# Optimization experiments

Measured on AMD Instinct MI355X. Metric: run time of the kernel, lower is better.

Reference implementation:

```python
import jax, jax.numpy as jnp
import numpy as np

N = 50000      # nodes
E = 1600000    # edges (avg degree 32)
F_IN = 128
HID = 256
C = 40


def setup_inputs() -> dict:
    key = jax.random.key(0)
    ks = jax.random.split(key, 12)
    x = jax.random.normal(ks[0], (N, F_IN), jnp.float32)
    edge_index = jax.random.randint(ks[1], (2, E), 0, N, dtype=jnp.int32)

    def glorot(k, fan_in, fan_out):
        s = jnp.sqrt(2.0 / (fan_in + fan_out)).astype(jnp.float32)
        return jax.random.normal(k, (fan_in, fan_out), jnp.float32) * s

    return {
        "x": x,
        "edge_index": edge_index,
        "W1": glorot(ks[2], F_IN, HID), "b1": jnp.zeros((HID,), jnp.float32),
        "W2": glorot(ks[3], HID, HID),  "b2": jnp.zeros((HID,), jnp.float32),
        "W3": glorot(ks[4], HID, HID),  "b3": jnp.zeros((HID,), jnp.float32),
        "W4": glorot(ks[5], HID, C),    "b4": jnp.zeros((C,), jnp.float32),
    }


def _gcn_conv(x, W, b, src, dst, norm_e, self_norm):
    # PyG GCNConv: h = X W; out_j = sum_i norm_ij * h_i  (+ self-loop term) + b
    h = x @ W                                   # [N, F_out]
    msg = h[src] * norm_e[:, None]              # [E, F_out] gather + scale
    agg = jax.ops.segment_sum(msg, dst, num_segments=N)
    agg = agg + h * self_norm[:, None]          # self-loop contribution
    return agg + b


def reference(x, edge_index, W1, b1, W2, b2, W3, b3, W4, b4):
    src, dst = edge_index[0], edge_index[1]
    # degree on A + I (self-loops added), computed over destination nodes
    deg = jax.ops.segment_sum(jnp.ones((E,), x.dtype), dst, num_segments=N) + 1.0
    inv_sqrt = jax.lax.rsqrt(deg)               # [N]
    norm_e = inv_sqrt[src] * inv_sqrt[dst]      # [E] symmetric norm per edge
    self_norm = inv_sqrt * inv_sqrt             # [N] self-loop norm = 1/deg

    h = jax.nn.relu(_gcn_conv(x, W1, b1, src, dst, norm_e, self_norm))
    h = jax.nn.relu(_gcn_conv(h, W2, b2, src, dst, norm_e, self_norm))
    h = jax.nn.relu(_gcn_conv(h, W3, b3, src, dst, norm_e, self_norm))
    h = _gcn_conv(h, W4, b4, src, dst, norm_e, self_norm)
    return jax.nn.log_softmax(h, axis=1)
```

## Files before the change

### kernel.cpp

```cpp
#include <hip/hip_runtime.h>
#include <hip/hip_fp16.h>
#include <math.h>


typedef _Float16 f16x8 __attribute__((ext_vector_type(8)));
typedef float f32x4 __attribute__((ext_vector_type(4)));
typedef unsigned u32x4 __attribute__((ext_vector_type(4)));

#define CAP 80

#define AS1 __attribute__((address_space(1)))
#define AS3 __attribute__((address_space(3)))

__device__ __forceinline__ void dma16(const unsigned short* g,
                                      const unsigned short* ldsBase) {
    __builtin_amdgcn_global_load_lds((const AS1 void*)(size_t)g,
                                     (AS3 void*)(unsigned)(size_t)ldsBase,
                                     16, 0, 0);
}

__device__ __forceinline__ __half2 u2h2(unsigned u) {
    union { unsigned u; __half2 h; } v; v.u = u; return v.h;
}
__device__ __forceinline__ unsigned h22u(__half2 h) {
    union { unsigned u; __half2 h; } v; v.h = h; return v.u;
}
__device__ __forceinline__ float hlo(unsigned u) {
    return __half2float(__ushort_as_half((unsigned short)(u & 0xFFFFu)));
}
__device__ __forceinline__ float hhi(unsigned u) {
    return __half2float(__ushort_as_half((unsigned short)(u >> 16)));
}

__global__ __launch_bounds__(256) void count_prep_kernel(
        const int* __restrict__ dst,
        int* __restrict__ cnt, int* __restrict__ rank, int E, int nEdgeBlocks,
        const float* __restrict__ x, unsigned short* __restrict__ xb, int nx4,
        const float* __restrict__ W1, const float* __restrict__ W2,
        const float* __restrict__ W3, const float* __restrict__ W4,
        unsigned short* __restrict__ Wt1, unsigned short* __restrict__ Wt2,
        unsigned short* __restrict__ Wt3, unsigned short* __restrict__ Wt4) {
    int b = blockIdx.x;
    if (b < nEdgeBlocks) {
        int e = b * 256 + threadIdx.x;
        if (e < E) rank[e] = atomicAdd(&cnt[dst[e]], 1);
        return;
    }
    int i = (b - nEdgeBlocks) * 256 + threadIdx.x;
    if (i < nx4) {
        float4 v = reinterpret_cast<const float4*>(x)[i];
        ushort4 o;
        o.x = __half_as_ushort(__float2half_rn(v.x));
        o.y = __half_as_ushort(__float2half_rn(v.y));
        o.z = __half_as_ushort(__float2half_rn(v.z));
        o.w = __half_as_ushort(__float2half_rn(v.w));
        reinterpret_cast<ushort4*>(xb)[i] = o;
        return;
    }
    int j = i - nx4;
    if (j < 32768) {
        int k = j >> 8, n = j & 255;
        Wt1[n * 128 + k] = __half_as_ushort(__float2half_rn(W1[j]));
    } else if (j < 98304) {
        int t = j - 32768; int k = t >> 8, n = t & 255;
        Wt2[n * 256 + k] = __half_as_ushort(__float2half_rn(W2[t]));
    } else if (j < 163840) {
        int t = j - 98304; int k = t >> 8, n = t & 255;
        Wt3[n * 256 + k] = __half_as_ushort(__float2half_rn(W3[t]));
    } else if (j < 174080) {
        int t = j - 163840; int k = t / 40, n = t - k * 40;
        Wt4[n * 256 + k] = __half_as_ushort(__float2half_rn(W4[t]));
    }
}

__global__ __launch_bounds__(256) void scatter_rsq_kernel(
        const int* __restrict__ src, const int* __restrict__ dst,
        const int* __restrict__ rank, unsigned short* __restrict__ epk,
        int E, int nEdgeBlocks,
        const int* __restrict__ cnt, float* __restrict__ rsq, int N) {
    int b = blockIdx.x;
    if (b < nEdgeBlocks) {
        int e = b * 256 + threadIdx.x;
        if (e < E) {
            int d = dst[e];
            int s = src[e];
            int r = rank[e]; if (r >= CAP) r = CAP - 1;
            epk[(size_t)d * CAP + r] = (unsigned short)s;
        }
        return;
    }
    int n = (b - nEdgeBlocks) * 256 + threadIdx.x;
    if (n < N) rsq[n] = rsqrtf((float)cnt[n] + 1.0f);
}

template <int ROWB, bool WSRC, bool BIAS, bool RELU>
__global__ __launch_bounds__(256) void agg_wide_kernel(
        const unsigned short* __restrict__ G,
        const int* __restrict__ cnt,
        const unsigned short* __restrict__ epk,
        const float* __restrict__ rsq,
        const float* __restrict__ bias,
        unsigned short* __restrict__ out, int N) {
    constexpr int ROWS = ROWB / 2;
    constexpr int LPN = ROWB / 16;
    constexpr int LOG_LPN = (LPN == 32) ? 5 : 4;
    constexpr int NPW = 64 / LPN;
    int lane = threadIdx.x & 63;
    int wid = threadIdx.x >> 6;
    int sub = lane >> LOG_LPN;
    int off = lane & (LPN - 1);
    int node = blockIdx.x * (4 * NPW) + wid * NPW + sub;
    if (node >= N) return;

    const unsigned short* gb = G + off * 8;
    const unsigned short* ep = epk + (size_t)node * CAP;
    int deg = cnt[node]; if (deg > CAP) deg = CAP;

    __half2 acc[4];
    #pragma unroll
    for (int k = 0; k < 4; k++) acc[k] = u2h2(0u);

    int e = 0;
    for (; e + 7 < deg; e += 8) {
        uint4 pv = *reinterpret_cast<const uint4*>(ep + e);
        int s[8];
        s[0] = pv.x & 0xFFFFu; s[1] = pv.x >> 16;
        s[2] = pv.y & 0xFFFFu; s[3] = pv.y >> 16;
        s[4] = pv.z & 0xFFFFu; s[5] = pv.z >> 16;
        s[6] = pv.w & 0xFFFFu; s[7] = pv.w >> 16;
        uint4 v[8];
        #pragma unroll
        for (int j = 0; j < 8; j++)
            v[j] = *reinterpret_cast<const uint4*>(gb + (size_t)s[j] * ROWS);
        if (WSRC) {
            float ws[8];
            #pragma unroll
            for (int j = 0; j < 8; j++) ws[j] = rsq[s[j]];
            #pragma unroll
            for (int j = 0; j < 8; j++) {
                __half2 w2 = __half2half2(__float2half_rn(ws[j]));
                acc[0] = __hfma2(w2, u2h2(v[j].x), acc[0]);
                acc[1] = __hfma2(w2, u2h2(v[j].y), acc[1]);
                acc[2] = __hfma2(w2, u2h2(v[j].z), acc[2]);
                acc[3] = __hfma2(w2, u2h2(v[j].w), acc[3]);
            }
        } else {
            #pragma unroll
            for (int j = 0; j < 8; j++) {
                acc[0] = __hadd2(acc[0], u2h2(v[j].x));
                acc[1] = __hadd2(acc[1], u2h2(v[j].y));
                acc[2] = __hadd2(acc[2], u2h2(v[j].z));
                acc[3] = __hadd2(acc[3], u2h2(v[j].w));
            }
        }
    }
    for (; e < deg; e++) {
        int s0 = ep[e];
        uint4 v0 = *reinterpret_cast<const uint4*>(gb + (size_t)s0 * ROWS);
        if (WSRC) {
            __half2 w2 = __half2half2(__float2half_rn(rsq[s0]));
            acc[0] = __hfma2(w2, u2h2(v0.x), acc[0]);
            acc[1] = __hfma2(w2, u2h2(v0.y), acc[1]);
            acc[2] = __hfma2(w2, u2h2(v0.z), acc[2]);
            acc[3] = __hfma2(w2, u2h2(v0.w), acc[3]);
        } else {
            acc[0] = __hadd2(acc[0], u2h2(v0.x));
            acc[1] = __hadd2(acc[1], u2h2(v0.y));
            acc[2] = __hadd2(acc[2], u2h2(v0.z));
            acc[3] = __hadd2(acc[3], u2h2(v0.w));
        }
    }

    float r = rsq[node];
    uint4 sv = *reinterpret_cast<const uint4*>(gb + (size_t)node * ROWS);
    unsigned svu[4] = {sv.x, sv.y, sv.z, sv.w};
    float sw = WSRC ? r : 1.0f;
    float r2 = r * r;
    u32x4 wp;
    float4 bv0, bv1;
    if (!WSRC && BIAS) {
        bv0 = reinterpret_cast<const float4*>(bias)[off * 2];
        bv1 = reinterpret_cast<const float4*>(bias)[off * 2 + 1];
    }
    float bvf[8] = {bv0.x, bv0.y, bv0.z, bv0.w, bv1.x, bv1.y, bv1.z, bv1.w};
    #pragma unroll
    for (int k = 0; k < 4; k++) {
        float2 f = __half22float2(acc[k]);
        f.x = fmaf(sw, hlo(svu[k]), f.x);
        f.y = fmaf(sw, hhi(svu[k]), f.y);
        float ox, oy;
        if (WSRC) {
            ox = r * f.x; oy = r * f.y;
        } else {
            ox = r2 * f.x; oy = r2 * f.y;
            if (BIAS) {
                ox = fmaf(r, bvf[2 * k], ox);
                oy = fmaf(r, bvf[2 * k + 1], oy);
            }
            if (RELU) { ox = fmaxf(ox, 0.f); oy = fmaxf(oy, 0.f); }
        }
        wp[k] = h22u(__floats2half2_rn(ox, oy));
    }
    __builtin_nontemporal_store(
        wp, reinterpret_cast<u32x4*>(out + (size_t)node * ROWS + off * 8));
}

__global__ __launch_bounds__(256) void agg40_softmax_kernel(
        const unsigned* __restrict__ G,
        const int* __restrict__ cnt,
        const unsigned short* __restrict__ epk,
        const float* __restrict__ rsq,
        const float* __restrict__ bias,
        float* __restrict__ out, int N) {
    int lane = threadIdx.x & 63;
    int node = blockIdx.x * 4 + (threadIdx.x >> 6);
    if (node >= N) return;
    bool act = lane < 20;
    int cl = act ? lane : 0;
    const unsigned short* ep = epk + (size_t)node * CAP;
    int deg = cnt[node]; if (deg > CAP) deg = CAP;
    __half2 acch = u2h2(0u);
    int e = 0;
    for (; e + 7 < deg; e += 8) {
        uint4 pv = *reinterpret_cast<const uint4*>(ep + e);
        int s[8];
        s[0] = pv.x & 0xFFFFu; s[1] = pv.x >> 16;
        s[2] = pv.y & 0xFFFFu; s[3] = pv.y >> 16;
        s[4] = pv.z & 0xFFFFu; s[5] = pv.z >> 16;
        s[6] = pv.w & 0xFFFFu; s[7] = pv.w >> 16;
        unsigned g[8];
        #pragma unroll
        for (int j = 0; j < 8; j++) g[j] = G[(size_t)s[j] * 20 + cl];
        #pragma unroll
        for (int j = 0; j < 8; j++) acch = __hadd2(acch, u2h2(g[j]));
    }
    for (; e < deg; e++) {
        int s0 = ep[e];
        acch = __hadd2(acch, u2h2(G[(size_t)s0 * 20 + cl]));
    }
    float lo = 0.f, hi = 0.f;
    if (act) {
        float r = rsq[node];
        unsigned sv = G[(size_t)node * 20 + lane];
        float2 f = __half22float2(acch);
        f.x += hlo(sv); f.y += hhi(sv);
        lo = fmaf(r, f.x, bias[2 * lane]);
        hi = fmaf(r, f.y, bias[2 * lane + 1]);
    }
    float m = act ? fmaxf(lo, hi) : -INFINITY;
    #pragma unroll
    for (int o = 32; o >= 1; o >>= 1) m = fmaxf(m, __shfl_xor(m, o, 64));
    float s = act ? (expf(lo - m) + expf(hi - m)) : 0.f;
    #pragma unroll
    for (int o = 32; o >= 1; o >>= 1) s += __shfl_xor(s, o, 64);
    float ls = logf(s);
    if (act) {
        float2 o2;
        o2.x = lo - m - ls;
        o2.y = hi - m - ls;
        *reinterpret_cast<float2*>(out + (size_t)node * 40 + 2 * lane) = o2;
    }
}

template <int BK, bool BIAS, bool RELU, bool SCALE>
__global__ __launch_bounds__(256) void gemm_f16(
        const unsigned short* __restrict__ A,
        const unsigned short* __restrict__ Bt,
        const float* __restrict__ bias,
        const float* __restrict__ rsqRow,
        unsigned short* __restrict__ Cout,
        int M, int K, int Nc) {
    constexpr int SPR = BK / 8;
    constexpr int NSTG = (128 * SPR) / 256;
    __shared__ __align__(16) unsigned short As[128 * BK];
    __shared__ __align__(16) unsigned short Bs[128 * BK];
    int tid = threadIdx.x;
    int lane = tid & 63;
    int wid = tid >> 6;
    int rowBase = blockIdx.y * 128;
    int colBase = blockIdx.x * 128;
    int waveM = (wid & 1) * 64;
    int waveN = (wid >> 1) * 64;

    f32x4 acc[4][4] = {};
    int lrow = lane & 15;
    int kgrp = (lane >> 4) * 8;

    for (int k0 = 0; k0 < K; k0 += BK) {
        #pragma unroll
        for (int c = 0; c < NSTG; c++) {
            int base16 = c * 256 + wid * 64;
            int slot = base16 + lane;
            int row = slot / SPR;
            int kp = (slot % SPR) * 8;
            int ksw = kp ^ ((row & (SPR - 1)) * 8);
            int gr = rowBase + row; if (gr >= M) gr = M - 1;
            dma16(A + (size_t)gr * K + k0 + ksw, &As[base16 * 8]);
            int gc = colBase + row; if (gc >= Nc) gc = Nc - 1;
            dma16(Bt + (size_t)gc * K + k0 + ksw, &Bs[base16 * 8]);
        }
        __syncthreads();
        #pragma unroll
        for (int kk = 0; kk < BK; kk += 32) {
            f16x8 af[4], bfr[4];
            #pragma unroll
            for (int t = 0; t < 4; t++) {
                int ra = waveM + t * 16 + lrow;
                af[t] = *reinterpret_cast<const f16x8*>(
                    &As[ra * BK + ((kk + kgrp) ^ ((ra & (SPR - 1)) * 8))]);
                int rb = waveN + t * 16 + lrow;
                bfr[t] = *reinterpret_cast<const f16x8*>(
                    &Bs[rb * BK + ((kk + kgrp) ^ ((rb & (SPR - 1)) * 8))]);
            }
            #pragma unroll
            for (int mt = 0; mt < 4; mt++)
                #pragma unroll
                for (int nt = 0; nt < 4; nt++)
                    acc[mt][nt] = __builtin_amdgcn_mfma_f32_16x16x32_f16(
                        af[mt], bfr[nt], acc[mt][nt], 0, 0, 0);
        }
        __syncthreads();
    }

    #pragma unroll
    for (int mt = 0; mt < 4; mt++) {
        #pragma unroll
        for (int r = 0; r < 4; r++) {
            int row = rowBase + waveM + mt * 16 + (lane >> 4) * 4 + r;
            if (row >= M) continue;
            float rs = SCALE ? rsqRow[row] : 1.0f;
            #pragma unroll
            for (int nt = 0; nt < 4; nt++) {
                int col = colBase + waveN + nt * 16 + (lane & 15);
                if (col >= Nc) continue;
                float v = acc[mt][nt][r];
                if (BIAS) v += bias[col];
                if (RELU) v = fmaxf(v, 0.f);
                if (SCALE) v *= rs;
                Cout[(size_t)row * Nc + col] = __half_as_ushort(__float2half_rn(v));
            }
        }
    }
}


extern "C" void kernel_launch(void* const* d_in, const int* in_sizes, int n_in,
                              void* d_out, int out_size, void* d_ws, size_t ws_size,
                              hipStream_t stream) {
    const float* x  = (const float*)d_in[0];
    const int*   ei = (const int*)d_in[1];
    const float* W1 = (const float*)d_in[2];
    const float* b1 = (const float*)d_in[3];
    const float* W2 = (const float*)d_in[4];
    const float* b2 = (const float*)d_in[5];
    const float* W3 = (const float*)d_in[6];
    const float* b3 = (const float*)d_in[7];
    const float* W4 = (const float*)d_in[8];
    const float* b4 = (const float*)d_in[9];

    const int FIN = 128, HID = 256, C = 40;
    const int N = in_sizes[0] / FIN;
    const int E = in_sizes[1] / 2;
    const int* src = ei;
    const int* dst = ei + E;

    char* w = (char*)d_ws;
    auto alloc = [&](size_t bytes) {
        char* p = w;
        w += (bytes + 255) & ~(size_t)255;
        return p;
    };
    int*   cnt    = (int*)alloc((size_t)N * 4);
    float* rsq    = (float*)alloc((size_t)N * 4);
    unsigned short* epk = (unsigned short*)alloc((size_t)N * CAP * 2);
    unsigned short* aggx = (unsigned short*)alloc((size_t)N * FIN * 2);
    unsigned short* bufA = (unsigned short*)alloc((size_t)N * HID * 2);
    unsigned short* bufB = (unsigned short*)alloc((size_t)N * HID * 2);
    unsigned short* Wt1 = (unsigned short*)alloc((size_t)FIN * HID * 2);
    unsigned short* Wt2 = (unsigned short*)alloc((size_t)HID * HID * 2);
    unsigned short* Wt3 = (unsigned short*)alloc((size_t)HID * HID * 2);
    unsigned short* Wt4 = (unsigned short*)alloc((size_t)HID * C * 2);
    unsigned short* xb = bufB;
    int* rank = (int*)aggx;

    hipMemsetAsync(cnt, 0, (size_t)N * 4, stream);

    int nx4 = N * FIN / 4;
    int nEdgeBlocks = (E + 255) / 256;
    int prepBlocks = (nx4 + 174080 + 255) / 256;
    count_prep_kernel<<<nEdgeBlocks + prepBlocks, 256, 0, stream>>>(
        dst, cnt, rank, E, nEdgeBlocks,
        x, xb, nx4, W1, W2, W3, W4, Wt1, Wt2, Wt3, Wt4);
    int rsqBlocks = (N + 255) / 256;
    scatter_rsq_kernel<<<nEdgeBlocks + rsqBlocks, 256, 0, stream>>>(
        src, dst, rank, epk, E, nEdgeBlocks, cnt, rsq, N);

    dim3 gAgg1((N + 15) / 16);
    dim3 gAggH((N + 7) / 8);
    int grp = (N + 3) / 4;
    dim3 gHID((HID + 127) / 128, (N + 127) / 128);
    dim3 gC((C + 127) / 128, (N + 127) / 128);

    agg_wide_kernel<256, true, false, false>
        <<<gAgg1, 256, 0, stream>>>(xb, cnt, epk, rsq, nullptr, aggx, N);
    gemm_f16<128, true, true, true><<<gHID, 256, 0, stream>>>(
        aggx, Wt1, b1, rsq, bufA, N, FIN, HID);
    gemm_f16<128, false, false, false><<<gHID, 256, 0, stream>>>(
        bufA, Wt2, nullptr, nullptr, bufB, N, HID, HID);
    agg_wide_kernel<512, false, true, true>
        <<<gAggH, 256, 0, stream>>>(bufB, cnt, epk, rsq, b2, bufA, N);
    gemm_f16<128, false, false, false><<<gHID, 256, 0, stream>>>(
        bufA, Wt3, nullptr, nullptr, bufB, N, HID, HID);
    agg_wide_kernel<512, false, true, true>
        <<<gAggH, 256, 0, stream>>>(bufB, cnt, epk, rsq, b3, bufA, N);
    gemm_f16<128, false, false, false><<<gC, 256, 0, stream>>>(
        bufA, Wt4, nullptr, nullptr, bufB, N, HID, C);
    agg40_softmax_kernel<<<grp, 256, 0, stream>>>((const unsigned*)bufB, cnt, epk,
                                                  rsq, b4, (float*)d_out, N);
}
```

Before: 577.3 us.

## Parallelize final 40-class aggregation across edges with LDS reduction

The final aggregation+log-softmax kernel previously used only 20 of 64 lanes, each gathering one half2 per edge serially. Now the wavefront processes 12 edges at once, each edge handled by 5 lanes doing 16-byte loads of the 40-half row, with per-lane partial sums reduced through shared memory. This raises memory-level parallelism and lane utilization for the gather, at the cost of an LDS round-trip and masked tail work. Summation order in fp16 changes slightly.

```diff
diff --git a/kernel.cpp b/kernel.cpp
--- a/kernel.cpp
+++ b/kernel.cpp
@@ -206,42 +206,51 @@
 }
 
 __global__ __launch_bounds__(256) void agg40_softmax_kernel(
-        const unsigned* __restrict__ G,
+        const unsigned short* __restrict__ G,
         const int* __restrict__ cnt,
         const unsigned short* __restrict__ epk,
         const float* __restrict__ rsq,
         const float* __restrict__ bias,
         float* __restrict__ out, int N) {
+    __shared__ __align__(16) unsigned red[4][64][4];
     int lane = threadIdx.x & 63;
-    int node = blockIdx.x * 4 + (threadIdx.x >> 6);
+    int wid = threadIdx.x >> 6;
+    int node = blockIdx.x * 4 + wid;
     if (node >= N) return;
-    bool act = lane < 20;
-    int cl = act ? lane : 0;
     const unsigned short* ep = epk + (size_t)node * CAP;
     int deg = cnt[node]; if (deg > CAP) deg = CAP;
+
+    int j = lane / 5;
+    int c = lane - j * 5;
+    __half2 a0 = u2h2(0u), a1 = u2h2(0u), a2 = u2h2(0u), a3 = u2h2(0u);
+    for (int e0 = 0; e0 < deg; e0 += 12) {
+        int e = e0 + j;
+        unsigned m = (j < 12 && e < deg) ? 0xFFFFFFFFu : 0u;
+        int ee = (e < deg) ? e : (deg - 1);
+        int s = ep[ee];
+        u32x4 v = *reinterpret_cast<const u32x4*>(G + (size_t)s * 40 + c * 8);
+        a0 = __hadd2(a0, u2h2(v.x & m));
+        a1 = __hadd2(a1, u2h2(v.y & m));
+        a2 = __hadd2(a2, u2h2(v.z & m));
+        a3 = __hadd2(a3, u2h2(v.w & m));
+    }
+    u32x4 packed;
+    packed.x = h22u(a0); packed.y = h22u(a1);
+    packed.z = h22u(a2); packed.w = h22u(a3);
+    *reinterpret_cast<u32x4*>(&red[wid][lane][0]) = packed;
+    bool act = lane < 20;
     __half2 acch = u2h2(0u);
-    int e = 0;
-    for (; e + 7 < deg; e += 8) {
-        uint4 pv = *reinterpret_cast<const uint4*>(ep + e);
-        int s[8];
-        s[0] = pv.x & 0xFFFFu; s[1] = pv.x >> 16;
-        s[2] = pv.y & 0xFFFFu; s[3] = pv.y >> 16;
-        s[4] = pv.z & 0xFFFFu; s[5] = pv.z >> 16;
-        s[6] = pv.w & 0xFFFFu; s[7] = pv.w >> 16;
-        unsigned g[8];
+    if (act) {
+        int cc = lane >> 2;
+        int w = lane & 3;
         #pragma unroll
-        for (int j = 0; j < 8; j++) g[j] = G[(size_t)s[j] * 20 + cl];
-        #pragma unroll
-        for (int j = 0; j < 8; j++) acch = __hadd2(acch, u2h2(g[j]));
-    }
-    for (; e < deg; e++) {
-        int s0 = ep[e];
-        acch = __hadd2(acch, u2h2(G[(size_t)s0 * 20 + cl]));
+        for (int jj = 0; jj < 12; jj++)
+            acch = __hadd2(acch, u2h2(red[wid][5 * jj + cc][w]));
     }
     float lo = 0.f, hi = 0.f;
     if (act) {
         float r = rsq[node];
-        unsigned sv = G[(size_t)node * 20 + lane];
+        unsigned sv = reinterpret_cast<const unsigned*>(G)[(size_t)node * 20 + lane];
         float2 f = __half22float2(acch);
         f.x += hlo(sv); f.y += hhi(sv);
         lo = fmaf(r, f.x, bias[2 * lane]);
@@ -415,6 +424,6 @@
         <<<gAggH, 256, 0, stream>>>(bufB, cnt, epk, rsq, b3, bufA, N);
     gemm_f16<128, false, false, false><<<gC, 256, 0, stream>>>(
         bufA, Wt4, nullptr, nullptr, bufB, N, HID, C);
-    agg40_softmax_kernel<<<grp, 256, 0, stream>>>((const unsigned*)bufB, cnt, epk,
+    agg40_softmax_kernel<<<grp, 256, 0, stream>>>(bufB, cnt, epk,
                                                   rsq, b4, (float*)d_out, N);
 }
```

Measured after the change: 562.6 us. -2.5%, faster.
